# Performance work log

Hardware: AMD Instinct MI355X
Metric: run time of the kernel (lower is better)

The kernel has to match this reference:

```python
import jax, jax.numpy as jnp
import numpy as np

BN_EPS = 1e-5

def conv1x1(x, w, b):
    # x: [b,c,h,w], w: [o,c], b: [o] -> [b,o,h,w]
    return jnp.einsum('bchw,oc->bohw', x, w) + b[None, :, None, None]

def setup_inputs() -> dict:
    key = jax.random.key(0)
    ks = jax.random.split(key, 12)
    C, Ci = 256, 128  # in_channels, inter_channels (ratio=2)
    B, H, W = 4, 56, 56
    s = 1.0 / np.sqrt(C)
    si = 1.0 / np.sqrt(Ci)
    return {
        'x':       jax.random.normal(ks[0], (B, C, H, W), jnp.float32),
        'w_theta': jax.random.normal(ks[1], (Ci, C), jnp.float32) * s,
        'b_theta': jax.random.normal(ks[2], (Ci,), jnp.float32) * s,
        'w_phi':   jax.random.normal(ks[3], (Ci, C), jnp.float32) * s,
        'b_phi':   jax.random.normal(ks[4], (Ci,), jnp.float32) * s,
        'w_g':     jax.random.normal(ks[5], (Ci, C), jnp.float32) * s,
        'b_g':     jax.random.normal(ks[6], (Ci,), jnp.float32) * s,
        'w_rec':   jax.random.normal(ks[7], (C, Ci), jnp.float32) * si,
        'b_rec':   jax.random.normal(ks[8], (C,), jnp.float32) * si,
        'bn_gamma': jax.random.normal(ks[9], (C,), jnp.float32) * 0.1 + 1.0,
        'bn_beta':  jax.random.normal(ks[10], (C,), jnp.float32) * 0.1,
        'bn_mean':  jax.random.normal(ks[11], (C,), jnp.float32) * 0.1,
        'bn_var':   jnp.ones((C,), jnp.float32),
    }

def reference(x, w_theta, b_theta, w_phi, b_phi, w_g, b_g,
              w_rec, b_rec, bn_gamma, bn_beta, bn_mean, bn_var):
    b, _, h, w = x.shape
    n = h * w
    c = w_theta.shape[0]  # inter_channels
    theta_x = conv1x1(x, w_theta, b_theta).reshape(b, c, n).transpose(0, 2, 1)  # [b,n,c]
    phi_x   = conv1x1(x, w_phi, b_phi).reshape(b, c, n)                         # [b,c,n]
    g_x     = conv1x1(x, w_g, b_g).reshape(b, c, n).transpose(0, 2, 1)          # [b,n,c]
    attention = jnp.matmul(theta_x, phi_x) / n                                  # [b,n,n]
    out = jnp.matmul(attention, g_x).transpose(0, 2, 1).reshape(b, c, h, w)
    out = conv1x1(out, w_rec, b_rec)
    # BatchNorm2d in inference form with given stats
    inv = bn_gamma / jnp.sqrt(bn_var + BN_EPS)
    out = out * inv[None, :, None, None] + (bn_beta - bn_mean * inv)[None, :, None, None]
    return out + x
```

## Files before the change

### kernel.cpp

```cpp
#include <hip/hip_runtime.h>

#define B 4
#define C 256
#define CI 128
#define NPIX 3136
#define KS 7
#define BN_EPS_F 1e-5f

typedef float f4 __attribute__((ext_vector_type(4)));
typedef float f32x4 __attribute__((ext_vector_type(4)));
typedef short short8 __attribute__((ext_vector_type(8)));
typedef short short4v __attribute__((ext_vector_type(4)));

__device__ inline short f2bf(float f) {
    unsigned u = __builtin_bit_cast(unsigned, f);
    unsigned r = (u + 0x7FFFu + ((u >> 16) & 1u)) >> 16;
    return (short)r;
}

__global__ __launch_bounds__(64) void rowsum_kernel(const float* __restrict__ x,
                                                    float* __restrict__ s) {
    int b = blockIdx.y, c = blockIdx.x;
    const float* row = x + ((size_t)(b * C + c)) * NPIX;
    float acc = 0.f;
    for (int n = threadIdx.x; n < NPIX; n += 64) acc += row[n];
#pragma unroll
    for (int off = 32; off > 0; off >>= 1) acc += __shfl_down(acc, off, 64);
    if (threadIdx.x == 0) s[b * C + c] = acc;
}

__global__ __launch_bounds__(256) void prep_kernel(const float* __restrict__ x,
                                                   short* __restrict__ xbf,
                                                   short* __restrict__ xT) {
    int b = blockIdx.z, c0 = blockIdx.y * 64, n0 = blockIdx.x * 64;
    __shared__ short lds[64][65];
    int t = threadIdx.x;
    int nf = (t & 15) * 4;
    int cr = t >> 4;
#pragma unroll
    for (int it = 0; it < 4; ++it) {
        int c = cr + 16 * it;
        f4 v = *(const f4*)&x[((size_t)(b * C + c0 + c)) * NPIX + n0 + nf];
        short4v s4;
#pragma unroll
        for (int i = 0; i < 4; ++i) s4[i] = f2bf(v[i]);
        *(short4v*)&xbf[((size_t)(b * C + c0 + c)) * NPIX + n0 + nf] = s4;
#pragma unroll
        for (int i = 0; i < 4; ++i) lds[nf + i][c] = s4[i];
    }
    __syncthreads();
#pragma unroll
    for (int it = 0; it < 4; ++it) {
        int n = cr + 16 * it;
        short4v s4;
#pragma unroll
        for (int i = 0; i < 4; ++i) s4[i] = lds[n][nf + i];
        *(short4v*)&xT[((size_t)b * NPIX + n0 + n) * C + c0 + nf] = s4;
    }
}

__global__ __launch_bounds__(256) void xxt_mfma(const short* __restrict__ xbf,
                                                float* __restrict__ Gp) {
    int z = blockIdx.z;
    int b = z / KS, ks = z % KS;
    int tid = threadIdx.x, lane = tid & 63, wid = tid >> 6;
    int ibase = blockIdx.y * 128 + (wid >> 1) * 64;
    int jbase = blockIdx.x * 128 + (wid & 1) * 64;
    int lm = lane & 15, lk = (lane >> 4) * 8;
    const short* A0 = xbf + ((size_t)(b * C) + ibase + lm) * NPIX + lk;
    const short* B0 = xbf + ((size_t)(b * C) + jbase + lm) * NPIX + lk;
    f32x4 acc[4][4] = {};
    int kend = ks * 448 + 448;
    for (int k = ks * 448; k < kend; k += 32) {
        short8 a[4], bv[4];
#pragma unroll
        for (int mi = 0; mi < 4; ++mi) a[mi] = *(const short8*)(A0 + (size_t)mi * 16 * NPIX + k);
#pragma unroll
        for (int nj = 0; nj < 4; ++nj) bv[nj] = *(const short8*)(B0 + (size_t)nj * 16 * NPIX + k);
#pragma unroll
        for (int mi = 0; mi < 4; ++mi)
#pragma unroll
            for (int nj = 0; nj < 4; ++nj)
                acc[mi][nj] = __builtin_amdgcn_mfma_f32_16x16x32_bf16(a[mi], bv[nj], acc[mi][nj], 0, 0, 0);
    }
    float* out = Gp + ((size_t)(ks * B + b)) * C * C;
    int r0 = (lane >> 4) * 4;
#pragma unroll
    for (int mi = 0; mi < 4; ++mi)
#pragma unroll
        for (int r = 0; r < 4; ++r)
#pragma unroll
            for (int nj = 0; nj < 4; ++nj)
                out[(ibase + mi * 16 + r0 + r) * C + jbase + nj * 16 + lm] = acc[mi][nj][r];
}

__global__ __launch_bounds__(256) void greduce_kernel(const float* __restrict__ Gp,
                                                      float* __restrict__ G) {
    int gid = blockIdx.x * 256 + threadIdx.x;
    float acc = 0.f;
#pragma unroll
    for (int ks = 0; ks < KS; ++ks) acc += Gp[(size_t)ks * (B * C * C) + gid];
    G[gid] = acc;
}

__global__ __launch_bounds__(256) void uv_kernel(const float* __restrict__ wphi,
                                                 const float* __restrict__ wg,
                                                 const float* __restrict__ s,
                                                 float* __restrict__ u,
                                                 float* __restrict__ v) {
    int b = blockIdx.x;
    __shared__ float sl[C];
    for (int i = threadIdx.x; i < C; i += 256) sl[i] = s[b * C + i];
    __syncthreads();
    int t = threadIdx.x;
    const float* wrow = (t < CI) ? (wphi + t * C) : (wg + (t - CI) * C);
    float acc = 0.f;
    for (int c = 0; c < C; ++c) acc += wrow[c] * sl[c];
    if (t < CI) u[b * CI + t] = acc;
    else        v[b * CI + (t - CI)] = acc;
}

__global__ __launch_bounds__(256) void pmat_kernel(const float* __restrict__ wphi,
                                                   const float* __restrict__ G,
                                                   float* __restrict__ P) {
    int gid = blockIdx.x * 256 + threadIdx.x;
    int b = gid >> 15;
    int i = (gid >> 8) & 127;
    int j = gid & 255;
    const float* wr = wphi + i * C;
    const float* Gb = G + (size_t)b * C * C;
    float acc = 0.f;
    for (int c = 0; c < C; ++c) acc += wr[c] * Gb[c * C + j];
    P[gid] = acc;
}

__global__ __launch_bounds__(256) void mmat_kernel(const float* __restrict__ P,
                                                   const float* __restrict__ wg,
                                                   const float* __restrict__ u,
                                                   const float* __restrict__ v,
                                                   const float* __restrict__ bphi,
                                                   const float* __restrict__ bg,
                                                   float* __restrict__ M) {
    int gid = blockIdx.x * 256 + threadIdx.x;
    int b = gid >> 14;
    int i = (gid >> 7) & 127;
    int j = gid & 127;
    const float* Pr = P + ((size_t)b * CI + i) * C;
    const float* wr = wg + j * C;
    float acc = 0.f;
    for (int c = 0; c < C; ++c) acc += Pr[c] * wr[c];
    const float invN = 1.0f / (float)NPIX;
    M[gid] = invN * (acc + u[b * CI + i] * bg[j] + bphi[i] * v[b * CI + j])
             + bphi[i] * bg[j];
}

__global__ __launch_bounds__(256) void amat_kernel(const float* __restrict__ wrec,
                                                   const float* __restrict__ M,
                                                   float* __restrict__ A) {
    int gid = blockIdx.x * 256 + threadIdx.x;
    int b = gid >> 15;
    int o = (gid >> 7) & 255;
    int i = gid & 127;
    const float* wr = wrec + o * CI;
    const float* Mb = M + (size_t)b * CI * CI;
    float acc = 0.f;
    for (int j = 0; j < CI; ++j) acc += wr[j] * Mb[i * CI + j];
    A[gid] = acc;
}

__global__ __launch_bounds__(256) void bias_kernel(const float* __restrict__ A,
                                                   const float* __restrict__ btheta,
                                                   const float* __restrict__ brec,
                                                   const float* __restrict__ gamma,
                                                   const float* __restrict__ beta,
                                                   const float* __restrict__ mean,
                                                   const float* __restrict__ var,
                                                   float* __restrict__ bias5) {
    int b = blockIdx.x, o = threadIdx.x;
    const float* Ar = A + ((size_t)b * C + o) * CI;
    float acc = 0.f;
    for (int i = 0; i < CI; ++i) acc += Ar[i] * btheta[i];
    float inv = gamma[o] * rsqrtf(var[o] + BN_EPS_F);
    bias5[b * C + o] = inv * (acc + brec[o]) + beta[o] - mean[o] * inv;
}

__global__ __launch_bounds__(256) void w5_kernel(const float* __restrict__ A,
                                                 const float* __restrict__ wtheta,
                                                 const float* __restrict__ gamma,
                                                 const float* __restrict__ var,
                                                 short* __restrict__ W5bf) {
    int gid = blockIdx.x * 256 + threadIdx.x;
    int b = gid >> 16;
    int o = (gid >> 8) & 255;
    int c = gid & 255;
    const float* Ar = A + ((size_t)b * C + o) * CI;
    float acc = 0.f;
    for (int i = 0; i < CI; ++i) acc += Ar[i] * wtheta[i * C + c];
    float inv = gamma[o] * rsqrtf(var[o] + BN_EPS_F);
    W5bf[gid] = f2bf(inv * acc);
}

__global__ __launch_bounds__(256) void final_mfma(const float* __restrict__ x,
                                                  const short* __restrict__ W5bf,
                                                  const short* __restrict__ xT,
                                                  const float* __restrict__ bias5,
                                                  float* __restrict__ out) {
    int b = blockIdx.y;
    int n0 = blockIdx.x * 64;
    int tid = threadIdx.x, lane = tid & 63, wid = tid >> 6;
    int obase = wid * 64;
    int lm = lane & 15, lk = (lane >> 4) * 8;
    const short* A0 = W5bf + ((size_t)(b * C) + obase + lm) * C + lk;
    const short* B0 = xT + ((size_t)b * NPIX + n0 + lm) * C + lk;
    f32x4 acc[4][4] = {};
#pragma unroll
    for (int k = 0; k < C; k += 32) {
        short8 a[4], bv[4];
#pragma unroll
        for (int mi = 0; mi < 4; ++mi) a[mi] = *(const short8*)(A0 + mi * 16 * C + k);
#pragma unroll
        for (int nj = 0; nj < 4; ++nj) bv[nj] = *(const short8*)(B0 + nj * 16 * C + k);
#pragma unroll
        for (int mi = 0; mi < 4; ++mi)
#pragma unroll
            for (int nj = 0; nj < 4; ++nj)
                acc[mi][nj] = __builtin_amdgcn_mfma_f32_16x16x32_bf16(a[mi], bv[nj], acc[mi][nj], 0, 0, 0);
    }
    int r0 = (lane >> 4) * 4;
#pragma unroll
    for (int mi = 0; mi < 4; ++mi) {
#pragma unroll
        for (int r = 0; r < 4; ++r) {
            int o = obase + mi * 16 + r0 + r;
            float bias = bias5[b * C + o];
            const float* xrow = x + ((size_t)(b * C + o)) * NPIX;
            float* orow = out + ((size_t)(b * C + o)) * NPIX;
#pragma unroll
            for (int nj = 0; nj < 4; ++nj) {
                int n = n0 + nj * 16 + lm;
                orow[n] = acc[mi][nj][r] + bias + xrow[n];
            }
        }
    }
}

extern "C" void kernel_launch(void* const* d_in, const int* in_sizes, int n_in,
                              void* d_out, int out_size, void* d_ws, size_t ws_size,
                              hipStream_t stream) {
    const float* x       = (const float*)d_in[0];
    const float* w_theta = (const float*)d_in[1];
    const float* b_theta = (const float*)d_in[2];
    const float* w_phi   = (const float*)d_in[3];
    const float* b_phi   = (const float*)d_in[4];
    const float* w_g     = (const float*)d_in[5];
    const float* b_g     = (const float*)d_in[6];
    const float* w_rec   = (const float*)d_in[7];
    const float* b_rec   = (const float*)d_in[8];
    const float* gamma   = (const float*)d_in[9];
    const float* beta    = (const float*)d_in[10];
    const float* mean    = (const float*)d_in[11];
    const float* var     = (const float*)d_in[12];
    float* out = (float*)d_out;

    float* Gp = out;
    float* G  = out + 1835008;
    float* P  = out + 2097152;
    float* M  = out + 2228224;
    float* A  = out + 2293760;

    char* wsb = (char*)d_ws;
    float* s     = (float*)(wsb + 0);
    float* u     = (float*)(wsb + 4096);
    float* v     = (float*)(wsb + 6144);
    float* bias5 = (float*)(wsb + 8192);
    short* W5bf  = (short*)(wsb + 16384);
    short* xbf   = (short*)(wsb + (1u << 20));
    short* xT    = (short*)(wsb + (8u << 20));

    rowsum_kernel<<<dim3(C, B), dim3(64), 0, stream>>>(x, s);
    prep_kernel<<<dim3(NPIX / 64, C / 64, B), dim3(256), 0, stream>>>(x, xbf, xT);
    xxt_mfma<<<dim3(2, 2, B * KS), dim3(256), 0, stream>>>(xbf, Gp);
    greduce_kernel<<<dim3(B * C * C / 256), dim3(256), 0, stream>>>(Gp, G);
    uv_kernel<<<dim3(B), dim3(256), 0, stream>>>(w_phi, w_g, s, u, v);
    pmat_kernel<<<dim3(B * CI * C / 256), dim3(256), 0, stream>>>(w_phi, G, P);
    mmat_kernel<<<dim3(B * CI * CI / 256), dim3(256), 0, stream>>>(P, w_g, u, v, b_phi, b_g, M);
    amat_kernel<<<dim3(B * C * CI / 256), dim3(256), 0, stream>>>(w_rec, M, A);
    bias_kernel<<<dim3(B), dim3(256), 0, stream>>>(A, b_theta, b_rec, gamma, beta, mean, var, bias5);
    w5_kernel<<<dim3(B * C * C / 256), dim3(256), 0, stream>>>(A, w_theta, gamma, var, W5bf);
    final_mfma<<<dim3(NPIX / 64, B), dim3(256), 0, stream>>>(x, W5bf, xT, bias5, out);
}
```

Measured before the change: 124.3 us.

## Reassociate small weight-chain matmuls into batch-independent L/R factors with tiled kernels

Restructures the small-matrix chain that builds the fused output weight. Batch-independent products (w_rec·w_g and w_phi^T·w_theta, plus bias vectors) are now precomputed once in a tiled LDS kernel. The per-batch work is reduced to two tiled GEMMs (L·G and H·R), with the partial-Gram reduction folded into the first one. The separate rowsum kernel is removed: row sums are now taken inside the prep kernel via shuffles and atomics, which adds a memset and atomic traffic. The intent is to cut kernel launches and the naive, uncoalesced per-thread dot-product kernels, at the cost of more complex bias algebra and a different float summation order.

```diff
diff --git a/kernel.cpp b/kernel.cpp
--- a/kernel.cpp
+++ b/kernel.cpp
@@ -6,6 +6,7 @@
 #define NPIX 3136
 #define KS 7
 #define BN_EPS_F 1e-5f
+#define INVN (1.0f / 3136.0f)
 
 typedef float f4 __attribute__((ext_vector_type(4)));
 typedef float f32x4 __attribute__((ext_vector_type(4)));
@@ -18,35 +19,35 @@
     return (short)r;
 }
 
-__global__ __launch_bounds__(64) void rowsum_kernel(const float* __restrict__ x,
-                                                    float* __restrict__ s) {
-    int b = blockIdx.y, c = blockIdx.x;
-    const float* row = x + ((size_t)(b * C + c)) * NPIX;
-    float acc = 0.f;
-    for (int n = threadIdx.x; n < NPIX; n += 64) acc += row[n];
-#pragma unroll
-    for (int off = 32; off > 0; off >>= 1) acc += __shfl_down(acc, off, 64);
-    if (threadIdx.x == 0) s[b * C + c] = acc;
-}
-
 __global__ __launch_bounds__(256) void prep_kernel(const float* __restrict__ x,
                                                    short* __restrict__ xbf,
-                                                   short* __restrict__ xT) {
+                                                   short* __restrict__ xT,
+                                                   float* __restrict__ s) {
     int b = blockIdx.z, c0 = blockIdx.y * 64, n0 = blockIdx.x * 64;
     __shared__ short lds[64][65];
     int t = threadIdx.x;
     int nf = (t & 15) * 4;
     int cr = t >> 4;
+    float psum[4];
 #pragma unroll
     for (int it = 0; it < 4; ++it) {
         int c = cr + 16 * it;
         f4 v = *(const f4*)&x[((size_t)(b * C + c0 + c)) * NPIX + n0 + nf];
         short4v s4;
-#pragma unroll
-        for (int i = 0; i < 4; ++i) s4[i] = f2bf(v[i]);
+        float ps = 0.f;
+#pragma unroll
+        for (int i = 0; i < 4; ++i) { s4[i] = f2bf(v[i]); ps += v[i]; }
+        psum[it] = ps;
         *(short4v*)&xbf[((size_t)(b * C + c0 + c)) * NPIX + n0 + nf] = s4;
 #pragma unroll
         for (int i = 0; i < 4; ++i) lds[nf + i][c] = s4[i];
+    }
+#pragma unroll
+    for (int it = 0; it < 4; ++it) {
+        float ps = psum[it];
+#pragma unroll
+        for (int m = 8; m >= 1; m >>= 1) ps += __shfl_xor(ps, m, 64);
+        if ((t & 15) == 0) atomicAdd(&s[b * C + c0 + cr + 16 * it], ps);
     }
     __syncthreads();
 #pragma unroll
@@ -56,6 +57,106 @@
 #pragma unroll
         for (int i = 0; i < 4; ++i) s4[i] = lds[n][nf + i];
         *(short4v*)&xT[((size_t)b * NPIX + n0 + n) * C + c0 + nf] = s4;
+    }
+}
+
+__global__ __launch_bounds__(256) void lr_kernel(const float* __restrict__ wrec,
+                                                 const float* __restrict__ wg,
+                                                 const float* __restrict__ wphi,
+                                                 const float* __restrict__ wtheta,
+                                                 const float* __restrict__ gamma,
+                                                 const float* __restrict__ var,
+                                                 const float* __restrict__ bg,
+                                                 const float* __restrict__ bphi,
+                                                 const float* __restrict__ btheta,
+                                                 const float* __restrict__ s,
+                                                 float* __restrict__ L,
+                                                 float* __restrict__ R,
+                                                 float* __restrict__ p,
+                                                 float* __restrict__ tg,
+                                                 float* __restrict__ wt,
+                                                 float* __restrict__ swt,
+                                                 float* __restrict__ consts) {
+    __shared__ float wl[64][68];
+    __shared__ float xl[64][68];
+    __shared__ float wtl[C];
+    int bx = blockIdx.x;
+    int t = threadIdx.x;
+    if (bx == 32) {
+        float acc_t = 0.f, acc_w = 0.f, accp = 0.f;
+        for (int j = 0; j < CI; ++j) {
+            float bp = bphi[j], bt = btheta[j];
+            acc_t += wtheta[j * C + t] * bp;
+            acc_w += wphi[j * C + t] * bt;
+            accp  += wrec[t * CI + j] * bg[j];
+        }
+        tg[t] = acc_t;
+        wt[t] = acc_w;
+        wtl[t] = acc_w;
+        p[t] = gamma[t] * rsqrtf(var[t] + BN_EPS_F) * accp;
+        __syncthreads();
+        if (t < B) {
+            float a = 0.f;
+            for (int c = 0; c < C; ++c) a += s[t * C + c] * wtl[c];
+            swt[t] = a;
+        }
+        if (t == 4) {
+            float a = 0.f;
+            for (int j = 0; j < CI; ++j) a += bphi[j] * btheta[j];
+            consts[0] = a;
+        }
+        return;
+    }
+    bool isL = bx < 16;
+    int bi = isL ? bx : bx - 16;
+    int r0 = (bi >> 2) * 64, cc0 = (bi & 3) * 64;
+    int tx = t & 15, ty = t >> 4;
+    float acc[4][4] = {};
+    for (int k0 = 0; k0 < CI; k0 += 64) {
+        __syncthreads();
+        if (isL) {
+#pragma unroll
+            for (int l = 0; l < 4; ++l) {
+                int idx = t + l * 256;
+                int r = idx >> 4, c4 = (idx & 15) << 2;
+                *(f4*)&wl[r][c4] = *(const f4*)&wrec[(r0 + r) * CI + k0 + c4];
+                *(f4*)&xl[r][c4] = *(const f4*)&wg[(size_t)(k0 + r) * C + cc0 + c4];
+            }
+        } else {
+#pragma unroll
+            for (int l = 0; l < 4; ++l) {
+                int idx = t + l * 256;
+                int jl = idx >> 4, cf4 = (idx & 15) << 2;
+                f4 v = *(const f4*)&wphi[(size_t)(k0 + jl) * C + r0 + cf4];
+#pragma unroll
+                for (int i = 0; i < 4; ++i) wl[cf4 + i][jl] = v[i];
+                *(f4*)&xl[jl][cf4] = *(const f4*)&wtheta[(size_t)(k0 + jl) * C + cc0 + cf4];
+            }
+        }
+        __syncthreads();
+        for (int kk = 0; kk < 64; kk += 4) {
+            f4 a[4], bb[4];
+#pragma unroll
+            for (int i = 0; i < 4; ++i) a[i] = *(const f4*)&wl[ty + 16 * i][kk];
+#pragma unroll
+            for (int q = 0; q < 4; ++q) bb[q] = *(const f4*)&xl[kk + q][tx * 4];
+#pragma unroll
+            for (int q = 0; q < 4; ++q)
+#pragma unroll
+                for (int i = 0; i < 4; ++i)
+#pragma unroll
+                    for (int j = 0; j < 4; ++j)
+                        acc[i][j] += a[i][q] * bb[q][j];
+        }
+    }
+#pragma unroll
+    for (int i = 0; i < 4; ++i) {
+        int r = r0 + ty + 16 * i;
+        float scale = isL ? gamma[r] * rsqrtf(var[r] + BN_EPS_F) : 1.0f;
+        float* dst = isL ? L : R;
+#pragma unroll
+        for (int j = 0; j < 4; ++j)
+            dst[r * C + cc0 + tx * 4 + j] = scale * acc[i][j];
     }
 }
 
@@ -83,7 +184,7 @@
             for (int nj = 0; nj < 4; ++nj)
                 acc[mi][nj] = __builtin_amdgcn_mfma_f32_16x16x32_bf16(a[mi], bv[nj], acc[mi][nj], 0, 0, 0);
     }
-    float* out = Gp + ((size_t)(ks * B + b)) * C * C;
+    float* outp = Gp + ((size_t)(ks * B + b)) * C * C;
     int r0 = (lane >> 4) * 4;
 #pragma unroll
     for (int mi = 0; mi < 4; ++mi)
@@ -91,113 +192,162 @@
         for (int r = 0; r < 4; ++r)
 #pragma unroll
             for (int nj = 0; nj < 4; ++nj)
-                out[(ibase + mi * 16 + r0 + r) * C + jbase + nj * 16 + lm] = acc[mi][nj][r];
-}
-
-__global__ __launch_bounds__(256) void greduce_kernel(const float* __restrict__ Gp,
-                                                      float* __restrict__ G) {
-    int gid = blockIdx.x * 256 + threadIdx.x;
-    float acc = 0.f;
-#pragma unroll
-    for (int ks = 0; ks < KS; ++ks) acc += Gp[(size_t)ks * (B * C * C) + gid];
-    G[gid] = acc;
-}
-
-__global__ __launch_bounds__(256) void uv_kernel(const float* __restrict__ wphi,
-                                                 const float* __restrict__ wg,
+                outp[(ibase + mi * 16 + r0 + r) * C + jbase + nj * 16 + lm] = acc[mi][nj][r];
+}
+
+__global__ __launch_bounds__(256) void h_kernel(const float* __restrict__ L,
+                                                const float* __restrict__ Gp,
+                                                const float* __restrict__ s,
+                                                float* __restrict__ H,
+                                                float* __restrict__ Ls) {
+    int jt = blockIdx.x, it = blockIdx.y, b = blockIdx.z;
+    int i0 = it * 64, j0 = jt * 64;
+    __shared__ float wl[64][68];
+    __shared__ float xl[64][68];
+    __shared__ float sl[C];
+    int t = threadIdx.x, tx = t & 15, ty = t >> 4;
+    sl[t] = s[b * C + t];
+    float acc[4][4] = {};
+    float lsacc[4] = {};
+    for (int k0 = 0; k0 < C; k0 += 64) {
+        __syncthreads();
+#pragma unroll
+        for (int l = 0; l < 4; ++l) {
+            int idx = t + l * 256;
+            int r = idx >> 4, c4 = (idx & 15) << 2;
+            *(f4*)&wl[r][c4] = *(const f4*)&L[(i0 + r) * C + k0 + c4];
+            f4 g = *(const f4*)&Gp[(size_t)b * C * C + (k0 + r) * C + j0 + c4];
+#pragma unroll
+            for (int ks = 1; ks < KS; ++ks)
+                g += *(const f4*)&Gp[(size_t)ks * (B * C * C) + (size_t)b * C * C + (k0 + r) * C + j0 + c4];
+            *(f4*)&xl[r][c4] = g;
+        }
+        __syncthreads();
+        for (int kk = 0; kk < 64; kk += 4) {
+            f4 a[4], bb[4];
+#pragma unroll
+            for (int i = 0; i < 4; ++i) a[i] = *(const f4*)&wl[ty + 16 * i][kk];
+#pragma unroll
+            for (int q = 0; q < 4; ++q) bb[q] = *(const f4*)&xl[kk + q][tx * 4];
+#pragma unroll
+            for (int q = 0; q < 4; ++q) {
+#pragma unroll
+                for (int i = 0; i < 4; ++i) {
+                    lsacc[i] += ((q == 0) ? a[i][0] * sl[k0 + kk] : 0.f);
+#pragma unroll
+                    for (int j = 0; j < 4; ++j)
+                        acc[i][j] += a[i][q] * bb[q][j];
+                }
+            }
+#pragma unroll
+            for (int i = 0; i < 4; ++i) {
+                lsacc[i] += a[i][1] * sl[k0 + kk + 1] + a[i][2] * sl[k0 + kk + 2] + a[i][3] * sl[k0 + kk + 3];
+            }
+        }
+    }
+    float* Hb = H + (size_t)b * C * C;
+#pragma unroll
+    for (int i = 0; i < 4; ++i)
+#pragma unroll
+        for (int j = 0; j < 4; ++j)
+            Hb[(i0 + ty + 16 * i) * C + j0 + tx * 4 + j] = acc[i][j];
+    if (jt == 0 && tx == 0) {
+#pragma unroll
+        for (int i = 0; i < 4; ++i) Ls[b * C + i0 + ty + 16 * i] = lsacc[i];
+    }
+}
+
+__global__ __launch_bounds__(256) void w5_kernel(const float* __restrict__ H,
+                                                 const float* __restrict__ R,
                                                  const float* __restrict__ s,
-                                                 float* __restrict__ u,
-                                                 float* __restrict__ v) {
-    int b = blockIdx.x;
-    __shared__ float sl[C];
-    for (int i = threadIdx.x; i < C; i += 256) sl[i] = s[b * C + i];
-    __syncthreads();
-    int t = threadIdx.x;
-    const float* wrow = (t < CI) ? (wphi + t * C) : (wg + (t - CI) * C);
-    float acc = 0.f;
-    for (int c = 0; c < C; ++c) acc += wrow[c] * sl[c];
-    if (t < CI) u[b * CI + t] = acc;
-    else        v[b * CI + (t - CI)] = acc;
-}
-
-__global__ __launch_bounds__(256) void pmat_kernel(const float* __restrict__ wphi,
-                                                   const float* __restrict__ G,
-                                                   float* __restrict__ P) {
-    int gid = blockIdx.x * 256 + threadIdx.x;
-    int b = gid >> 15;
-    int i = (gid >> 8) & 127;
-    int j = gid & 255;
-    const float* wr = wphi + i * C;
-    const float* Gb = G + (size_t)b * C * C;
-    float acc = 0.f;
-    for (int c = 0; c < C; ++c) acc += wr[c] * Gb[c * C + j];
-    P[gid] = acc;
-}
-
-__global__ __launch_bounds__(256) void mmat_kernel(const float* __restrict__ P,
-                                                   const float* __restrict__ wg,
-                                                   const float* __restrict__ u,
-                                                   const float* __restrict__ v,
-                                                   const float* __restrict__ bphi,
-                                                   const float* __restrict__ bg,
-                                                   float* __restrict__ M) {
-    int gid = blockIdx.x * 256 + threadIdx.x;
-    int b = gid >> 14;
-    int i = (gid >> 7) & 127;
-    int j = gid & 127;
-    const float* Pr = P + ((size_t)b * CI + i) * C;
-    const float* wr = wg + j * C;
-    float acc = 0.f;
-    for (int c = 0; c < C; ++c) acc += Pr[c] * wr[c];
-    const float invN = 1.0f / (float)NPIX;
-    M[gid] = invN * (acc + u[b * CI + i] * bg[j] + bphi[i] * v[b * CI + j])
-             + bphi[i] * bg[j];
-}
-
-__global__ __launch_bounds__(256) void amat_kernel(const float* __restrict__ wrec,
-                                                   const float* __restrict__ M,
-                                                   float* __restrict__ A) {
-    int gid = blockIdx.x * 256 + threadIdx.x;
-    int b = gid >> 15;
-    int o = (gid >> 7) & 255;
-    int i = gid & 127;
-    const float* wr = wrec + o * CI;
-    const float* Mb = M + (size_t)b * CI * CI;
-    float acc = 0.f;
-    for (int j = 0; j < CI; ++j) acc += wr[j] * Mb[i * CI + j];
-    A[gid] = acc;
-}
-
-__global__ __launch_bounds__(256) void bias_kernel(const float* __restrict__ A,
-                                                   const float* __restrict__ btheta,
-                                                   const float* __restrict__ brec,
-                                                   const float* __restrict__ gamma,
-                                                   const float* __restrict__ beta,
-                                                   const float* __restrict__ mean,
-                                                   const float* __restrict__ var,
-                                                   float* __restrict__ bias5) {
-    int b = blockIdx.x, o = threadIdx.x;
-    const float* Ar = A + ((size_t)b * C + o) * CI;
-    float acc = 0.f;
-    for (int i = 0; i < CI; ++i) acc += Ar[i] * btheta[i];
-    float inv = gamma[o] * rsqrtf(var[o] + BN_EPS_F);
-    bias5[b * C + o] = inv * (acc + brec[o]) + beta[o] - mean[o] * inv;
-}
-
-__global__ __launch_bounds__(256) void w5_kernel(const float* __restrict__ A,
-                                                 const float* __restrict__ wtheta,
+                                                 const float* __restrict__ wt,
+                                                 const float* __restrict__ tg,
+                                                 const float* __restrict__ p,
+                                                 const float* __restrict__ Ls,
+                                                 const float* __restrict__ swt,
+                                                 const float* __restrict__ consts,
                                                  const float* __restrict__ gamma,
                                                  const float* __restrict__ var,
-                                                 short* __restrict__ W5bf) {
-    int gid = blockIdx.x * 256 + threadIdx.x;
-    int b = gid >> 16;
-    int o = (gid >> 8) & 255;
-    int c = gid & 255;
-    const float* Ar = A + ((size_t)b * C + o) * CI;
-    float acc = 0.f;
-    for (int i = 0; i < CI; ++i) acc += Ar[i] * wtheta[i * C + c];
-    float inv = gamma[o] * rsqrtf(var[o] + BN_EPS_F);
-    W5bf[gid] = f2bf(inv * acc);
+                                                 const float* __restrict__ beta,
+                                                 const float* __restrict__ mean,
+                                                 const float* __restrict__ brec,
+                                                 short* __restrict__ W5bf,
+                                                 float* __restrict__ bias5) {
+    int jt = blockIdx.x, it = blockIdx.y, b = blockIdx.z;
+    int o0 = it * 64, c0 = jt * 64;
+    __shared__ float wl[64][68];
+    __shared__ float xl[64][68];
+    __shared__ float sl[C];
+    __shared__ float wtl[C];
+    int t = threadIdx.x, tx = t & 15, ty = t >> 4;
+    sl[t] = s[b * C + t];
+    wtl[t] = wt[t];
+    float acc[4][4] = {};
+    float qacc[4] = {};
+    float hwacc[4] = {};
+    const float* Hb = H + (size_t)b * C * C;
+    for (int k0 = 0; k0 < C; k0 += 64) {
+        __syncthreads();
+#pragma unroll
+        for (int l = 0; l < 4; ++l) {
+            int idx = t + l * 256;
+            int r = idx >> 4, c4 = (idx & 15) << 2;
+            *(f4*)&wl[r][c4] = *(const f4*)&Hb[(o0 + r) * C + k0 + c4];
+            *(f4*)&xl[r][c4] = *(const f4*)&R[(k0 + r) * C + c0 + c4];
+        }
+        __syncthreads();
+        for (int kk = 0; kk < 64; kk += 4) {
+            f4 a[4], bb[4];
+#pragma unroll
+            for (int i = 0; i < 4; ++i) a[i] = *(const f4*)&wl[ty + 16 * i][kk];
+#pragma unroll
+            for (int q = 0; q < 4; ++q) bb[q] = *(const f4*)&xl[kk + q][tx * 4];
+#pragma unroll
+            for (int q = 0; q < 4; ++q) {
+                float sq = sl[k0 + kk + q], wq = wtl[k0 + kk + q];
+#pragma unroll
+                for (int i = 0; i < 4; ++i) {
+                    hwacc[i] += a[i][q] * wq;
+#pragma unroll
+                    for (int j = 0; j < 4; ++j)
+                        acc[i][j] += a[i][q] * bb[q][j];
+                }
+#pragma unroll
+                for (int j = 0; j < 4; ++j) qacc[j] += sq * bb[q][j];
+            }
+        }
+    }
+    float tj[4], qj[4];
+#pragma unroll
+    for (int j = 0; j < 4; ++j) {
+        tj[j] = tg[c0 + tx * 4 + j];
+        qj[j] = INVN * qacc[j] + tj[j];
+    }
+    short* Wb = W5bf + (size_t)b * C * C;
+#pragma unroll
+    for (int i = 0; i < 4; ++i) {
+        int o = o0 + ty + 16 * i;
+        float pi = p[o];
+        float lsi = Ls[b * C + o];
+#pragma unroll
+        for (int j = 0; j < 4; ++j) {
+            float w5v = INVN * acc[i][j] + pi * qj[j] + INVN * lsi * tj[j];
+            Wb[o * C + c0 + tx * 4 + j] = f2bf(w5v);
+        }
+    }
+    if (jt == 0 && tx == 0) {
+        float swtb = swt[b];
+        float cpt = consts[0];
+#pragma unroll
+        for (int i = 0; i < 4; ++i) {
+            int o = o0 + ty + 16 * i;
+            float inv_o = gamma[o] * rsqrtf(var[o] + BN_EPS_F);
+            float pi = p[o];
+            bias5[b * C + o] = INVN * hwacc[i] + INVN * swtb * pi
+                             + cpt * (INVN * Ls[b * C + o] + pi)
+                             + inv_o * brec[o] + beta[o] - mean[o] * inv_o;
+        }
+    }
 }
 
 __global__ __launch_bounds__(256) void final_mfma(const float* __restrict__ x,
@@ -263,29 +413,32 @@
     float* out = (float*)d_out;
 
     float* Gp = out;
-    float* G  = out + 1835008;
-    float* P  = out + 2097152;
-    float* M  = out + 2228224;
-    float* A  = out + 2293760;
+    float* H  = out + 1835008;
 
     char* wsb = (char*)d_ws;
-    float* s     = (float*)(wsb + 0);
-    float* u     = (float*)(wsb + 4096);
-    float* v     = (float*)(wsb + 6144);
-    float* bias5 = (float*)(wsb + 8192);
-    short* W5bf  = (short*)(wsb + 16384);
-    short* xbf   = (short*)(wsb + (1u << 20));
-    short* xT    = (short*)(wsb + (8u << 20));
-
-    rowsum_kernel<<<dim3(C, B), dim3(64), 0, stream>>>(x, s);
-    prep_kernel<<<dim3(NPIX / 64, C / 64, B), dim3(256), 0, stream>>>(x, xbf, xT);
+    float* s      = (float*)(wsb + 0);
+    float* swt    = (float*)(wsb + 4096);
+    float* consts = (float*)(wsb + 4160);
+    float* p      = (float*)(wsb + 8192);
+    float* tg     = (float*)(wsb + 12288);
+    float* wt     = (float*)(wsb + 16384);
+    float* Ls     = (float*)(wsb + 20480);
+    float* bias5  = (float*)(wsb + 24576);
+    float* L      = (float*)(wsb + 32768);
+    float* R      = (float*)(wsb + 294912);
+    short* W5bf   = (short*)(wsb + 557056);
+    short* xbf    = (short*)(wsb + (2u << 20));
+    short* xT     = (short*)(wsb + (16u << 20));
+
+    hipMemsetAsync(s, 0, B * C * sizeof(float), stream);
+    prep_kernel<<<dim3(NPIX / 64, C / 64, B), dim3(256), 0, stream>>>(x, xbf, xT, s);
+    lr_kernel<<<dim3(33), dim3(256), 0, stream>>>(w_rec, w_g, w_phi, w_theta,
+                                                  gamma, var, b_g, b_phi, b_theta,
+                                                  s, L, R, p, tg, wt, swt, consts);
     xxt_mfma<<<dim3(2, 2, B * KS), dim3(256), 0, stream>>>(xbf, Gp);
-    greduce_kernel<<<dim3(B * C * C / 256), dim3(256), 0, stream>>>(Gp, G);
-    uv_kernel<<<dim3(B), dim3(256), 0, stream>>>(w_phi, w_g, s, u, v);
-    pmat_kernel<<<dim3(B * CI * C / 256), dim3(256), 0, stream>>>(w_phi, G, P);
-    mmat_kernel<<<dim3(B * CI * CI / 256), dim3(256), 0, stream>>>(P, w_g, u, v, b_phi, b_g, M);
-    amat_kernel<<<dim3(B * C * CI / 256), dim3(256), 0, stream>>>(w_rec, M, A);
-    bias_kernel<<<dim3(B), dim3(256), 0, stream>>>(A, b_theta, b_rec, gamma, beta, mean, var, bias5);
-    w5_kernel<<<dim3(B * C * C / 256), dim3(256), 0, stream>>>(A, w_theta, gamma, var, W5bf);
+    h_kernel<<<dim3(4, 4, B), dim3(256), 0, stream>>>(L, Gp, s, H, Ls);
+    w5_kernel<<<dim3(4, 4, B), dim3(256), 0, stream>>>(H, R, s, wt, tg, p, Ls, swt, consts,
+                                                       gamma, var, beta, mean, b_rec,
+                                                       W5bf, bias5);
     final_mfma<<<dim3(NPIX / 64, B), dim3(256), 0, stream>>>(x, W5bf, xT, bias5, out);
 }
```

Result: slower. 175.7 us (+41.3%).
